# Kernel tuning notes

Hardware: AMD Instinct MI355X
Metric: run time of the kernel (lower is better)

## Reference

```python
import jax, jax.numpy as jnp
import numpy as np

B, S, D, H = 1, 4096, 1024, 16
HD = D // H

def _w(k, std):
    return jax.random.truncated_normal(k, -3.0, 3.0, (D, D), jnp.float32) * std

def setup_inputs() -> dict:
    key = jax.random.key(0)
    kx, kq, kk, kv, ko = jax.random.split(key, 5)
    std = (2.0 / (D + D)) ** 0.5
    return {
        "x": jax.random.normal(kx, (B, S, D), jnp.float32),
        "Wq": _w(kq, std),
        "Wk": _w(kk, std),
        "Wv": _w(kv, std),
        "Wo": _w(ko, std),
    }

def reference(x, Wq, Wk, Wv, Wo):
    # projections: Linear applies W [d_out, d_in] as x @ W.T
    def split_heads(t):
        return t.reshape(B, S, H, HD).transpose(0, 2, 1, 3)  # [B,H,S,hd]
    q = split_heads(jnp.einsum('bsd,ed->bse', x, Wq))
    k = split_heads(jnp.einsum('bsd,ed->bse', x, Wk))
    v = split_heads(jnp.einsum('bsd,ed->bse', x, Wv))
    scores = jnp.einsum('bhqd,bhkd->bhqk', q, k) / (HD ** 0.5)  # [B,H,S,S]
    causal = jnp.tril(jnp.ones((S, S), bool))
    scores = jnp.where(causal, scores, -jnp.inf)
    attn = jax.nn.softmax(scores, axis=-1)
    out = jnp.einsum('bhqk,bhkd->bhqd', attn, v)  # [B,H,S,hd]
    out = out.transpose(0, 2, 1, 3).reshape(B, S, D)
    return jnp.einsum('bsd,ed->bse', out, Wo)
```

## Files before the change

kernel.cpp:

```cpp
#include <hip/hip_runtime.h>
#include <hip/hip_bf16.h>
#include <stdint.h>

constexpr int SEQ  = 4096;
constexpr int DIM  = 1024;
constexpr int NH   = 16;
constexpr int HDM  = 64;

typedef __bf16 bf16;
typedef __attribute__((ext_vector_type(4)))  float  f32x4;
typedef __attribute__((ext_vector_type(16))) float  f32x16;
typedef __attribute__((ext_vector_type(8)))  __bf16 bf16x8;
typedef __attribute__((ext_vector_type(4)))  __bf16 bf16x4;
typedef __attribute__((ext_vector_type(4)))  unsigned u32x4;

__device__ __forceinline__ void gload_lds16(const bf16* g, bf16* l) {
  __builtin_amdgcn_global_load_lds(
      (const __attribute__((address_space(1))) unsigned int*)g,
      (__attribute__((address_space(3))) unsigned int*)l, 16, 0, 0);
}

__device__ __forceinline__ unsigned pack2(float lo, float hi) {
  unsigned short a = __builtin_bit_cast(unsigned short, (bf16)lo);
  unsigned short b = __builtin_bit_cast(unsigned short, (bf16)hi);
  return ((unsigned)b << 16) | a;
}

__global__ void cvt5(const float* __restrict__ x,  const float* __restrict__ wq,
                     const float* __restrict__ wk, const float* __restrict__ wv,
                     const float* __restrict__ wo,
                     bf16* __restrict__ xb,  bf16* __restrict__ wqb,
                     bf16* __restrict__ wkb, bf16* __restrict__ wvb,
                     bf16* __restrict__ wob) {
  const float* in; bf16* out; int n;
  switch (blockIdx.y) {
    case 0:  in = x;  out = xb;  n = SEQ * DIM; break;
    case 1:  in = wq; out = wqb; n = DIM * DIM; break;
    case 2:  in = wk; out = wkb; n = DIM * DIM; break;
    case 3:  in = wv; out = wvb; n = DIM * DIM; break;
    default: in = wo; out = wob; n = DIM * DIM; break;
  }
  const int i = (blockIdx.x * blockDim.x + threadIdx.x) * 8;
  if (i >= n) return;
  f32x4 a = *(const f32x4*)(in + i);
  f32x4 b = *(const f32x4*)(in + i + 4);
  bf16x8 o;
#pragma unroll
  for (int j = 0; j < 4; ++j) { o[j] = (bf16)a[j]; o[j + 4] = (bf16)b[j]; }
  *(bf16x8*)(out + i) = o;
}

template <typename OutT, bool QKV>
__global__ __launch_bounds__(256, 2)
void gemm_xwt(const bf16* __restrict__ A,
              const bf16* __restrict__ W0, const bf16* __restrict__ W1,
              const bf16* __restrict__ W2,
              OutT* __restrict__ C0, OutT* __restrict__ C1, OutT* __restrict__ C2) {
  const bf16* W;
  OutT* C;
  float sc = 1.0f;
  if (QKV) {
    const int z = blockIdx.z;
    W = (z == 0) ? W0 : (z == 1) ? W1 : W2;
    C = (z == 0) ? C0 : (z == 1) ? C1 : C2;
    if (z == 0) sc = 0.18033688011112042f;
  } else {
    W = W0; C = C0;
  }
  __shared__ bf16 As[128 * 32];
  __shared__ bf16 Bs[128 * 32];
  const int tid = threadIdx.x;
  const int w   = tid >> 6;
  const int l   = tid & 63;
  const int l15 = l & 15, lhi = l >> 4;
  const int wr  = w >> 1, wc = w & 1;
  const int row0 = blockIdx.y * 128;
  const int col0 = blockIdx.x * 128;

  f32x4 acc[4][4] = {};

  const int srow = w * 32 + (l >> 2);
  const int scol = (l & 3) * 8;
  const bf16* gA = A + (size_t)(row0 + srow) * DIM + scol;
  const bf16* gB = W + (size_t)(col0 + srow) * DIM + scol;
  bf16* lA = As + srow * 32 + scol;
  bf16* lB = Bs + srow * 32 + scol;

  for (int k0 = 0; k0 < DIM; k0 += 32) {
    __syncthreads();
    gload_lds16(gA + k0,            lA);
    gload_lds16(gA + k0 + 16 * DIM, lA + 16 * 32);
    gload_lds16(gB + k0,            lB);
    gload_lds16(gB + k0 + 16 * DIM, lB + 16 * 32);
    __syncthreads();
    bf16x8 af[4], bf_[4];
#pragma unroll
    for (int m = 0; m < 4; ++m)
      af[m] = *(const bf16x8*)(As + (wr * 64 + m * 16 + l15) * 32 + lhi * 8);
#pragma unroll
    for (int n = 0; n < 4; ++n)
      bf_[n] = *(const bf16x8*)(Bs + (wc * 64 + n * 16 + l15) * 32 + lhi * 8);
#pragma unroll
    for (int m = 0; m < 4; ++m)
#pragma unroll
      for (int n = 0; n < 4; ++n)
        acc[m][n] = __builtin_amdgcn_mfma_f32_16x16x32_bf16(af[m], bf_[n], acc[m][n], 0, 0, 0);
  }

#pragma unroll
  for (int m = 0; m < 4; ++m)
#pragma unroll
    for (int n = 0; n < 4; ++n)
#pragma unroll
      for (int r = 0; r < 4; ++r) {
        const int row = row0 + wr * 64 + m * 16 + lhi * 4 + r;
        const int col = col0 + wc * 64 + n * 16 + l15;
        C[(size_t)row * DIM + col] = (OutT)(acc[m][n][r] * sc);
      }
}

__global__ __launch_bounds__(256)
void transpose_v(const bf16* __restrict__ Vs, bf16* __restrict__ Vt) {
  __shared__ bf16 t[64][72];
  const int st = blockIdx.x * 64;
  const int dt = blockIdx.y * 64;
  const int tid = threadIdx.x;
  const int r  = tid >> 2;
  const int c0 = (tid & 3) * 16;
  bf16x8 a = *(const bf16x8*)(Vs + (size_t)(st + r) * DIM + dt + c0);
  bf16x8 b = *(const bf16x8*)(Vs + (size_t)(st + r) * DIM + dt + c0 + 8);
#pragma unroll
  for (int j = 0; j < 8; ++j) { t[r][c0 + j] = a[j]; t[r][c0 + 8 + j] = b[j]; }
  __syncthreads();
  const int d  = tid >> 2;
  const int s0 = (tid & 3) * 16;
  bf16x8 o1, o2;
#pragma unroll
  for (int j = 0; j < 8; ++j) { o1[j] = t[s0 + j][d]; o2[j] = t[s0 + 8 + j][d]; }
  bf16* dst = Vt + (size_t)(dt + d) * SEQ + st + s0;
  *(bf16x8*)(dst)     = o1;
  *(bf16x8*)(dst + 8) = o2;
}

__global__ __launch_bounds__(256, 2)
void attn_fwd(const bf16* __restrict__ Qg, const bf16* __restrict__ Kg,
              const bf16* __restrict__ Vt,
              bf16* __restrict__ P0, bf16* __restrict__ P1,
              bf16* __restrict__ P2, bf16* __restrict__ P3,
              float* __restrict__ ms) {
  __shared__ bf16 Kl[2][8][64][8];
  __shared__ bf16 Vl[2][8][64][8];
  const int tid = threadIdx.x;
  const int wv  = tid >> 6;
  const int l   = tid & 63;
  const int l31 = l & 31;
  const int hi  = l >> 5;
  const int bid = blockIdx.x;
  const int s   = bid & 3;
  const int bh  = bid >> 2;
  const int b   = 31 - (bh >> 4);
  const int h   = bh & 15;
  const int qb0 = b * 128;
  const int hc  = h * HDM;
  const int tmaxb = 2 * b + 1;
  const int tdiag = 2 * b + (wv >> 1);
  const int qg  = qb0 + wv * 32 + l31;
  bf16* Po = (s == 0) ? P0 : (s == 1) ? P1 : (s == 2) ? P2 : P3;

  bf16x8 qf[4];
#pragma unroll
  for (int ks = 0; ks < 4; ++ks)
    qf[ks] = *(const bf16x8*)(Qg + (size_t)qg * DIM + hc + ks * 16 + hi * 8);

  f32x16 ot0 = {}, ot1 = {};
  float sacc[8] = {};

  auto stage = [&](int bb, int t) {
    const int kv0 = t * 64;
#pragma unroll
    for (int c = 0; c < 2; ++c) {
      const int p = c * 4 + wv;
      gload_lds16(Kg + (size_t)(kv0 + l) * DIM + hc + p * 8, &Kl[bb][p][0][0]);
      gload_lds16(Vt + (size_t)(hc + l) * SEQ + kv0 + p * 8, &Vl[bb][p][0][0]);
    }
  };

  if (s <= tmaxb) {
    stage(0, s);
    int bb = 0;
#pragma unroll 1
    for (int t = s; t <= tmaxb; t += 4) {
      __syncthreads();
      if (t + 4 <= tmaxb) stage(bb ^ 1, t + 4);
      if (t <= tdiag) {
        const int kv0 = t * 64;
        bf16x8 kf0[4], kf1[4];
#pragma unroll
        for (int ks = 0; ks < 4; ++ks) {
          kf0[ks] = *(const bf16x8*)&Kl[bb][ks * 2 + hi][l31][0];
          kf1[ks] = *(const bf16x8*)&Kl[bb][ks * 2 + hi][32 + l31][0];
        }
        f32x16 s0 = {}, s1 = {};
        __builtin_amdgcn_s_setprio(1);
#pragma unroll
        for (int ks = 0; ks < 4; ++ks) {
          s0 = __builtin_amdgcn_mfma_f32_32x32x16_bf16(kf0[ks], qf[ks], s0, 0, 0, 0);
          s1 = __builtin_amdgcn_mfma_f32_32x32x16_bf16(kf1[ks], qf[ks], s1, 0, 0, 0);
        }
        __builtin_amdgcn_s_setprio(0);
        bf16x8 vf0[4], vf1[4];
#pragma unroll
        for (int k2 = 0; k2 < 4; ++k2) {
          vf0[k2] = *(const bf16x8*)&Vl[bb][k2 * 2 + hi][l31][0];
          vf1[k2] = *(const bf16x8*)&Vl[bb][k2 * 2 + hi][32 + l31][0];
        }
        if (t == tdiag) {
#pragma unroll
          for (int r = 0; r < 16; ++r) {
            const int kp = (r & 3) + 8 * (r >> 2) + 4 * hi;
            if (kv0 + kp      > qg) s0[r] = -1.0e30f;
            if (kv0 + 32 + kp > qg) s1[r] = -1.0e30f;
          }
        }
#pragma unroll
        for (int r = 0; r < 16; ++r) {
          s0[r] = __builtin_exp2f(s0[r]);
          s1[r] = __builtin_exp2f(s1[r]);
        }
#pragma unroll
        for (int r = 0; r < 8; ++r)
          sacc[r] += (s0[r] + s0[r + 8]) + (s1[r] + s1[r + 8]);
        __builtin_amdgcn_s_setprio(1);
#pragma unroll
        for (int sub = 0; sub < 2; ++sub) {
#pragma unroll
          for (int hf = 0; hf < 2; ++hf) {
            const int rb = hf * 8;
            float v0, v1, v2, v3, v4, v5, v6, v7;
            if (sub == 0) {
              v0 = s0[rb+0]; v1 = s0[rb+1]; v2 = s0[rb+2]; v3 = s0[rb+3];
              v4 = s0[rb+4]; v5 = s0[rb+5]; v6 = s0[rb+6]; v7 = s0[rb+7];
            } else {
              v0 = s1[rb+0]; v1 = s1[rb+1]; v2 = s1[rb+2]; v3 = s1[rb+3];
              v4 = s1[rb+4]; v5 = s1[rb+5]; v6 = s1[rb+6]; v7 = s1[rb+7];
            }
            const unsigned w0 = pack2(v0, v1), w1 = pack2(v2, v3);
            const unsigned w2 = pack2(v4, v5), w3 = pack2(v6, v7);
            const unsigned sa = hi ? w0 : w2;
            const unsigned sb = hi ? w1 : w3;
            const unsigned ra  = (unsigned)__shfl_xor((int)sa, 32);
            const unsigned rb_ = (unsigned)__shfl_xor((int)sb, 32);
            u32x4 fu;
            fu[0] = hi ? ra  : w0;
            fu[1] = hi ? rb_ : w1;
            fu[2] = hi ? w2  : ra;
            fu[3] = hi ? w3  : rb_;
            const bf16x8 pb = __builtin_bit_cast(bf16x8, fu);
            const int k2 = sub * 2 + hf;
            ot0 = __builtin_amdgcn_mfma_f32_32x32x16_bf16(
                k2 == 0 ? vf0[0] : k2 == 1 ? vf0[1] : k2 == 2 ? vf0[2] : vf0[3],
                pb, ot0, 0, 0, 0);
            ot1 = __builtin_amdgcn_mfma_f32_32x32x16_bf16(
                k2 == 0 ? vf1[0] : k2 == 1 ? vf1[1] : k2 == 2 ? vf1[2] : vf1[3],
                pb, ot1, 0, 0, 0);
          }
        }
        __builtin_amdgcn_s_setprio(0);
      }
      bb ^= 1;
    }
  }

  float sum_ = 0.f;
  {
    float t4[4];
#pragma unroll
    for (int r = 0; r < 4; ++r) t4[r] = sacc[r] + sacc[r + 4];
    sum_ = (t4[0] + t4[1]) + (t4[2] + t4[3]);
    sum_ += __shfl_xor(sum_, 32);
  }
#pragma unroll
  for (int g = 0; g < 4; ++g) {
    bf16x4 o0, o1;
#pragma unroll
    for (int e = 0; e < 4; ++e) {
      o0[e] = (bf16)ot0[g * 4 + e];
      o1[e] = (bf16)ot1[g * 4 + e];
    }
    *(bf16x4*)(Po + (size_t)qg * DIM + hc + g * 8 + hi * 4)      = o0;
    *(bf16x4*)(Po + (size_t)qg * DIM + hc + 32 + g * 8 + hi * 4) = o1;
  }
  if (hi == 0)
    ms[((size_t)s * SEQ + qg) * NH + h] = sum_;
}

__global__ __launch_bounds__(256)
void attn_combine(const bf16* __restrict__ P0, const bf16* __restrict__ P1,
                  const bf16* __restrict__ P2, const bf16* __restrict__ P3,
                  const float* __restrict__ ms, bf16* __restrict__ At) {
  const int idx = blockIdx.x * 256 + threadIdx.x;
  const int q  = idx >> 7;
  const int d0 = (idx & 127) * 8;
  const int h  = d0 >> 6;
  float den = 0.f;
#pragma unroll
  for (int s = 0; s < 4; ++s)
    den += ms[((size_t)s * SEQ + q) * NH + h];
  const float inv = 1.0f / den;
  const size_t off = (size_t)q * DIM + d0;
  bf16x8 p0 = *(const bf16x8*)(P0 + off);
  bf16x8 p1 = *(const bf16x8*)(P1 + off);
  bf16x8 p2 = *(const bf16x8*)(P2 + off);
  bf16x8 p3 = *(const bf16x8*)(P3 + off);
  bf16x8 o;
#pragma unroll
  for (int j = 0; j < 8; ++j) {
    const float v = (float)p0[j] + (float)p1[j] + (float)p2[j] + (float)p3[j];
    o[j] = (bf16)(v * inv);
  }
  *(bf16x8*)(At + off) = o;
}

extern "C" void kernel_launch(void* const* d_in, const int* in_sizes, int n_in,
                              void* d_out, int out_size, void* d_ws, size_t ws_size,
                              hipStream_t stream) {
  const float* x  = (const float*)d_in[0];
  const float* Wq = (const float*)d_in[1];
  const float* Wk = (const float*)d_in[2];
  const float* Wv = (const float*)d_in[3];
  const float* Wo = (const float*)d_in[4];
  float* out = (float*)d_out;

  constexpr size_t MT = (size_t)SEQ * DIM;
  bf16* xb  = (bf16*)d_ws;
  bf16* wqb = xb  + MT;
  bf16* wkb = wqb + (size_t)DIM * DIM;
  bf16* wvb = wkb + (size_t)DIM * DIM;
  bf16* wob = wvb + (size_t)DIM * DIM;
  bf16* Qs  = wob + (size_t)DIM * DIM;
  bf16* Ks  = Qs  + MT;
  bf16* Vs  = Ks  + MT;
  bf16* P1  = Vs  + MT;
  bf16* P2  = P1  + MT;
  bf16* P3  = P2  + MT;
  float* ms = (float*)(P3 + MT);
  bf16* Vt  = xb;
  bf16* P0  = Vs;
  bf16* At  = Vs;

  cvt5<<<dim3((SEQ * DIM) / (256 * 8), 5), 256, 0, stream>>>(
      x, Wq, Wk, Wv, Wo, xb, wqb, wkb, wvb, wob);

  gemm_xwt<bf16, true><<<dim3(DIM / 128, SEQ / 128, 3), 256, 0, stream>>>(
      xb, wqb, wkb, wvb, Qs, Ks, Vs);

  transpose_v<<<dim3(SEQ / 64, DIM / 64), 256, 0, stream>>>(Vs, Vt);

  attn_fwd<<<dim3(2048), 256, 0, stream>>>(Qs, Ks, Vt, P0, P1, P2, P3, ms);

  attn_combine<<<dim3((SEQ * DIM / 8) / 256), 256, 0, stream>>>(
      P0, P1, P2, P3, ms, At);

  gemm_xwt<float, false><<<dim3(DIM / 128, SEQ / 128), 256, 0, stream>>>(
      At, wob, nullptr, nullptr, out, nullptr, nullptr);
}
```

Baseline: 154.2 us.

## Split PV accumulators for MFMA ILP and use smaller-tile output GEMM

In the attention kernel, the P·V accumulation now goes into two independent accumulator pairs, chosen by sub-block, and they are summed at the end. This breaks the serial MFMA dependency chain so consecutive MFMAs can overlap, at the cost of 32 extra accumulator registers per lane. The output projection switches to a new 64x128-tile GEMM kernel with launch bounds of 2 waves per SIMD. That doubles the grid from 256 to 512 blocks to fill more CUs, at the cost of less reuse per tile.

```diff
diff --git a/kernel.cpp b/kernel.cpp
--- a/kernel.cpp
+++ b/kernel.cpp
@@ -116,6 +116,61 @@
         const int row = row0 + wr * 64 + m * 16 + lhi * 4 + r;
         const int col = col0 + wc * 64 + n * 16 + l15;
         C[(size_t)row * DIM + col] = (OutT)(acc[m][n][r] * sc);
+      }
+}
+
+__global__ __launch_bounds__(256, 2)
+void gemm_out(const bf16* __restrict__ A, const bf16* __restrict__ W,
+              float* __restrict__ C) {
+  __shared__ bf16 As[64 * 32];
+  __shared__ bf16 Bs[128 * 32];
+  const int tid = threadIdx.x;
+  const int w   = tid >> 6;
+  const int l   = tid & 63;
+  const int l15 = l & 15, lhi = l >> 4;
+  const int wr  = w >> 1, wc = w & 1;
+  const int row0 = blockIdx.y * 64;
+  const int col0 = blockIdx.x * 128;
+
+  f32x4 acc[2][4] = {};
+
+  const int srowA = w * 16 + (l >> 2);
+  const int srowB = w * 32 + (l >> 2);
+  const int scol  = (l & 3) * 8;
+  const bf16* gA = A + (size_t)(row0 + srowA) * DIM + scol;
+  const bf16* gB = W + (size_t)(col0 + srowB) * DIM + scol;
+  bf16* lA = As + srowA * 32 + scol;
+  bf16* lB = Bs + srowB * 32 + scol;
+
+  for (int k0 = 0; k0 < DIM; k0 += 32) {
+    __syncthreads();
+    gload_lds16(gA + k0,            lA);
+    gload_lds16(gB + k0,            lB);
+    gload_lds16(gB + k0 + 16 * DIM, lB + 16 * 32);
+    __syncthreads();
+    bf16x8 af[2], bf_[4];
+#pragma unroll
+    for (int m = 0; m < 2; ++m)
+      af[m] = *(const bf16x8*)(As + (wr * 32 + m * 16 + l15) * 32 + lhi * 8);
+#pragma unroll
+    for (int n = 0; n < 4; ++n)
+      bf_[n] = *(const bf16x8*)(Bs + (wc * 64 + n * 16 + l15) * 32 + lhi * 8);
+#pragma unroll
+    for (int m = 0; m < 2; ++m)
+#pragma unroll
+      for (int n = 0; n < 4; ++n)
+        acc[m][n] = __builtin_amdgcn_mfma_f32_16x16x32_bf16(af[m], bf_[n], acc[m][n], 0, 0, 0);
+  }
+
+#pragma unroll
+  for (int m = 0; m < 2; ++m)
+#pragma unroll
+    for (int n = 0; n < 4; ++n)
+#pragma unroll
+      for (int r = 0; r < 4; ++r) {
+        const int row = row0 + wr * 32 + m * 16 + lhi * 4 + r;
+        const int col = col0 + wc * 64 + n * 16 + l15;
+        C[(size_t)row * DIM + col] = acc[m][n][r];
       }
 }
 
@@ -172,7 +227,7 @@
   for (int ks = 0; ks < 4; ++ks)
     qf[ks] = *(const bf16x8*)(Qg + (size_t)qg * DIM + hc + ks * 16 + hi * 8);
 
-  f32x16 ot0 = {}, ot1 = {};
+  f32x16 ota0 = {}, otb0 = {}, ota1 = {}, otb1 = {};
   float sacc[8] = {};
 
   auto stage = [&](int bb, int t) {
@@ -256,13 +311,17 @@
             fu[2] = hi ? w2  : ra;
             fu[3] = hi ? w3  : rb_;
             const bf16x8 pb = __builtin_bit_cast(bf16x8, fu);
-            const int k2 = sub * 2 + hf;
-            ot0 = __builtin_amdgcn_mfma_f32_32x32x16_bf16(
-                k2 == 0 ? vf0[0] : k2 == 1 ? vf0[1] : k2 == 2 ? vf0[2] : vf0[3],
-                pb, ot0, 0, 0, 0);
-            ot1 = __builtin_amdgcn_mfma_f32_32x32x16_bf16(
-                k2 == 0 ? vf1[0] : k2 == 1 ? vf1[1] : k2 == 2 ? vf1[2] : vf1[3],
-                pb, ot1, 0, 0, 0);
+            const bf16x8 va0 = (sub == 0) ? (hf == 0 ? vf0[0] : vf0[1])
+                                          : (hf == 0 ? vf0[2] : vf0[3]);
+            const bf16x8 va1 = (sub == 0) ? (hf == 0 ? vf1[0] : vf1[1])
+                                          : (hf == 0 ? vf1[2] : vf1[3]);
+            if (sub == 0) {
+              ota0 = __builtin_amdgcn_mfma_f32_32x32x16_bf16(va0, pb, ota0, 0, 0, 0);
+              ota1 = __builtin_amdgcn_mfma_f32_32x32x16_bf16(va1, pb, ota1, 0, 0, 0);
+            } else {
+              otb0 = __builtin_amdgcn_mfma_f32_32x32x16_bf16(va0, pb, otb0, 0, 0, 0);
+              otb1 = __builtin_amdgcn_mfma_f32_32x32x16_bf16(va1, pb, otb1, 0, 0, 0);
+            }
           }
         }
         __builtin_amdgcn_s_setprio(0);
@@ -271,6 +330,9 @@
     }
   }
 
+  f32x16 ot0, ot1;
+#pragma unroll
+  for (int r = 0; r < 16; ++r) { ot0[r] = ota0[r] + otb0[r]; ot1[r] = ota1[r] + otb1[r]; }
   float sum_ = 0.f;
   {
     float t4[4];
@@ -361,6 +423,5 @@
   attn_combine<<<dim3((SEQ * DIM / 8) / 256), 256, 0, stream>>>(
       P0, P1, P2, P3, ms, At);
 
-  gemm_xwt<float, false><<<dim3(DIM / 128, SEQ / 128), 256, 0, stream>>>(
-      At, wob, nullptr, nullptr, out, nullptr, nullptr);
-}
+  gemm_out<<<dim3(DIM / 128, SEQ / 64), 256, 0, stream>>>(At, wob, out);
+}
```

New measurement: 157.5 us. +2.1%, slower.
